# Kernel optimization log

Hardware: AMD Instinct MI355X
Metric: run time of the kernel (lower is better)

Reference implementation:

```python
import jax, jax.numpy as jnp
import numpy as np

T, B, N = 12, 2, 1024
M = B * N            # nodes per timestep (batch-flattened)
D_IN, D_H, D_T, D_O = 64, 128, 16, 32


def _linear_params(k, fin, fout):
    kw, kb = jax.random.split(k)
    s = 1.0 / np.sqrt(fin)
    w = jax.random.uniform(kw, (fin, fout), jnp.float32, -s, s)
    b = jax.random.uniform(kb, (fout,), jnp.float32, -s, s)
    return w, b


def setup_inputs() -> dict:
    key = jax.random.key(0)
    ks = jax.random.split(key, 12)
    x = jax.random.normal(ks[0], (T, M, D_IN), jnp.float32)
    A = (jax.random.uniform(ks[1], (T, M, M)) < 0.01).astype(jnp.float32)
    A = A * (1.0 - jnp.eye(M, dtype=jnp.float32))  # no self-loops in raw adjacency
    ego_mask = jax.random.randint(ks[2], (B, T, N), 0, 2).astype(bool)
    gcn1_w, gcn1_b = _linear_params(ks[3], D_IN, D_H)
    gcn2_w, gcn2_b = _linear_params(ks[4], D_H, D_H)
    time_w, time_b = _linear_params(ks[5], 1, D_T)
    q_w, q_b = _linear_params(ks[6], D_H + D_T, D_H)
    k_w, k_b = _linear_params(ks[7], D_H + D_T, D_H)
    v_w, v_b = _linear_params(ks[8], D_H + D_T, D_H)
    o_w, o_b = _linear_params(ks[9], D_H, D_H)
    fc_w, fc_b = _linear_params(ks[10], D_H, D_O)
    return dict(x=x, A=A, ego_mask=ego_mask,
                gcn1_w=gcn1_w, gcn1_b=gcn1_b, gcn2_w=gcn2_w, gcn2_b=gcn2_b,
                time_w=time_w, time_b=time_b,
                q_w=q_w, q_b=q_b, k_w=k_w, k_b=k_b, v_w=v_w, v_b=v_b,
                o_w=o_w, o_b=o_b, fc_w=fc_w, fc_b=fc_b)


def _forward(x, A, ego_mask, gcn1_w, gcn1_b, gcn2_w, gcn2_b, time_w, time_b,
             q_w, q_b, k_w, k_b, v_w, v_b, o_w, o_b, fc_w, fc_b):
    # [B,T,N] -> [T, B*N], as in mask.permute(1,0,2).reshape(T,-1)
    mask = ego_mask.transpose(1, 0, 2).reshape(T, M)
    tvals = jnp.arange(T, dtype=jnp.float32)

    def step(_, inp):
        xt, At, mt, tv = inp  # [M,D_IN], [M,M], [M] bool, scalar
        m = mt.astype(xt.dtype)
        # restrict adjacency to masked subgraph; GCNConv adds self-loops
        A_hat = At * (m[:, None] * m[None, :]) + jnp.diag(m)
        deg = A_hat.sum(axis=0)  # in-degree per target (PyG gcn_norm on col)
        nrm = jnp.where(deg > 0, 1.0 / jnp.sqrt(jnp.maximum(deg, 1e-12)), 0.0)

        def gcn(h, w, b):
            # out[i] = nrm[i] * sum_j A_hat[j,i] * nrm[j] * (hW)[j] + b
            return (A_hat.T @ ((h @ w) * nrm[:, None])) * nrm[:, None] + b

        h = jax.nn.relu(gcn(xt, gcn1_w, gcn1_b))
        h = jax.nn.relu(gcn(h, gcn2_w, gcn2_b))
        # t_vec = sin(Linear(1,D_T)(t)) -- identical for all nodes
        t_vec = jnp.sin(tv * time_w[0] + time_b)  # [D_T]
        xtc = jnp.concatenate([h, jnp.broadcast_to(t_vec, (M, D_T))], axis=-1)
        Q = xtc @ q_w + q_b
        K = xtc @ k_w + k_b
        V = xtc @ v_w + v_b
        scores = (Q @ K.T) * (1.0 / np.sqrt(D_H))  # [M,M]
        scores = jnp.where(mt[None, :], scores, -1e9)  # keys restricted to mask
        agg = jax.nn.softmax(scores, axis=-1) @ V
        out = ((agg @ o_w + o_b) @ fc_w + fc_b) * m[:, None]  # scatter-back == mask
        return None, out

    _, outs = jax.lax.scan(step, None, (x, A, mask, tvals))  # [T,M,D_O]
    return outs.reshape(T, B, N, D_O).transpose(1, 2, 0, 3)  # [B,N,T,D_O]


def reference(x, A, ego_mask, gcn1_w, gcn1_b, gcn2_w, gcn2_b, time_w, time_b,
              q_w, q_b, k_w, k_b, v_w, v_b, o_w, o_b, fc_w, fc_b):
    return _forward(x, A, ego_mask, gcn1_w, gcn1_b, gcn2_w, gcn2_b, time_w,
                    time_b, q_w, q_b, k_w, k_b, v_w, v_b, o_w, o_b, fc_w, fc_b)
```

## Files before the change

### kernel.cpp

```cpp
#include <hip/hip_runtime.h>
#include <stdint.h>

#define TT   12
#define BB   2
#define NN   1024
#define MM   2048
#define TM   24576
#define DIN  64
#define DH   128
#define DOUT 32
#define CAP  64
#define NSPL 4
#define OUTSZ 786432

typedef __attribute__((ext_vector_type(8))) short short8;
typedef __attribute__((ext_vector_type(4))) short short4v;
typedef __attribute__((ext_vector_type(4))) float f32x4;

#define MFMA(a,b,c) __builtin_amdgcn_mfma_f32_16x16x32_bf16((a),(b),(c),0,0,0)

__device__ __forceinline__ float bf2f(unsigned short u){
  union { uint32_t i; float f; } x; x.i = ((uint32_t)u) << 16; return x.f;
}
__device__ __forceinline__ unsigned short f2bf(float f){
  union { float f; uint32_t i; } x; x.f = f;
  uint32_t u = x.i + 0x7FFFu + ((x.i >> 16) & 1u);
  return (unsigned short)(u >> 16);
}
__device__ __forceinline__ float LD(const void* p, size_t i, int mode){
  return mode ? ((const float*)p)[i] : bf2f(((const unsigned short*)p)[i]);
}
__device__ __forceinline__ short8 ldx8(const void* x, size_t off, int md){
  if(md){
    const float4* xf = (const float4*)((const float*)x + off);
    float4 a = xf[0], b = xf[1];
    short8 o;
    o[0]=(short)f2bf(a.x); o[1]=(short)f2bf(a.y); o[2]=(short)f2bf(a.z); o[3]=(short)f2bf(a.w);
    o[4]=(short)f2bf(b.x); o[5]=(short)f2bf(b.y); o[6]=(short)f2bf(b.z); o[7]=(short)f2bf(b.w);
    return o;
  }
  return *(const short8*)((const unsigned short*)x + off);
}

__global__ void k_fill(float* __restrict__ out, int n, float val){
  int i = blockIdx.x*blockDim.x + threadIdx.x;
  if(i < n) out[i] = val;
}

__global__ void k_detect2(const unsigned short* __restrict__ x,
                          const unsigned char* __restrict__ eg,
                          int* __restrict__ dtf, int* __restrict__ flag,
                          int* __restrict__ nact){
  if(blockIdx.x == 0){
    __shared__ int cnt_s;
    if(threadIdx.x==0) cnt_s = 0;
    if(threadIdx.x < TT) nact[threadIdx.x] = 0;
    __syncthreads();
    int c = 0;
    for(int i=threadIdx.x; i<6144; i+=blockDim.x){
      unsigned short h = x[i*2];
      unsigned e = (h >> 7) & 0xFF;
      if(h==0 || (e >= 0x60 && e <= 0x9F)) c++;
    }
    atomicAdd(&cnt_s, c);
    __syncthreads();
    if(threadIdx.x==0) *dtf = (cnt_s > 4000) ? 0 : 1;
  } else {
    __shared__ int pres_s, ge2_s;
    if(threadIdx.x==0){ pres_s=0; ge2_s=0; }
    __syncthreads();
    int pres=0, ge2=0;
    for(int i=threadIdx.x; i<24576; i+=blockDim.x){
      unsigned v = eg[i];
      if(v){ pres |= 1 << (i & 7); if(v >= 2u) ge2 = 1; }
    }
    if(pres) atomicOr(&pres_s, pres);
    if(ge2)  atomicOr(&ge2_s, 1);
    __syncthreads();
    if(threadIdx.x==0){
      int pr = pres_s, g2 = ge2_s, mode;
      if(!g2){
        if((pr & ~0x01) == 0)      mode = 4;
        else if((pr & ~0x11) == 0) mode = 0;
        else                       mode = 1;
      } else {
        if((pr & ~0xC0) == 0)      mode = 5;
        else if((pr & ~0xCC) == 0) mode = 3;
        else                       mode = 2;
      }
      *flag = mode;
    }
  }
}

__global__ void k_mask(const void* __restrict__ egom, const int* __restrict__ flag,
                       int* __restrict__ cnt, int* __restrict__ nact,
                       int* __restrict__ aidx, int* __restrict__ inv,
                       float* __restrict__ out){
  int idx = blockIdx.x*blockDim.x + threadIdx.x;
  out[idx] = 0.f;
  if(idx >= TM) return;
  int t = idx / MM, node = idx % MM;
  int b = node / NN, n = node % NN;
  int src = (b*TT + t)*NN + n;
  int mode = *flag;
  int v;
  if(mode==0)      v = ((const int*)egom)[src] != 0;
  else if(mode==1) v = ((const unsigned char*)egom)[src] != 0;
  else if(mode==2) v = ((const unsigned short*)egom)[src] != 0;
  else if(mode==3) v = ((const float*)egom)[src] != 0.f;
  else if(mode==4) v = ((const long long*)egom)[src] != 0;
  else             v = ((const double*)egom)[src] != 0.0;
  cnt[idx] = 0;
  unsigned long long bal = __ballot(v != 0);
  int lane = threadIdx.x & 63;
  int base = 0;
  if(lane == 0 && bal) base = atomicAdd(&nact[t], __popcll(bal));
  base = __shfl(base, 0, 64);
  int ic = -1;
  if(v){
    int pfx = __popcll(bal & ((1ULL << lane) - 1ULL));
    ic = base + pfx;
    aidx[(size_t)t*MM + ic] = node;
  }
  inv[idx] = ic;
}

__global__ void k_prepw(
  const void* __restrict__ w1, const void* __restrict__ w2,
  const void* __restrict__ qw, const void* __restrict__ kw, const void* __restrict__ vw,
  const void* __restrict__ qb0, const void* __restrict__ kb0, const void* __restrict__ vb0,
  const void* __restrict__ ow, const void* __restrict__ ob,
  const void* __restrict__ fw, const void* __restrict__ fb,
  const void* __restrict__ tw, const void* __restrict__ tb,
  const void* __restrict__ b1, const void* __restrict__ b2,
  const int* __restrict__ dtf,
  unsigned short* __restrict__ W1t, unsigned short* __restrict__ W2t,
  unsigned short* __restrict__ Wqt, unsigned short* __restrict__ Wkt,
  unsigned short* __restrict__ Wvt, unsigned short* __restrict__ Wct,
  float* __restrict__ qbf, float* __restrict__ kbf, float* __restrict__ vbf,
  float* __restrict__ bcf, float* __restrict__ b1f, float* __restrict__ b2f)
{
  const int md = *dtf;
  int id = blockIdx.x*blockDim.x + threadIdx.x;
  if(id < 8192){
    int n=id&127, k2=id>>7; W1t[n*64+k2]=f2bf(LD(w1,(size_t)k2*128+n,md)); return; }
  id -= 8192;
  if(id < 16384){ int n=id&127,k2=id>>7; W2t[n*128+k2]=f2bf(LD(w2,(size_t)k2*128+n,md)); return; }
  id -= 16384;
  if(id < 16384){ int n=id&127,k2=id>>7; Wqt[n*128+k2]=f2bf(LD(qw,(size_t)k2*128+n,md)); return; }
  id -= 16384;
  if(id < 16384){ int n=id&127,k2=id>>7; Wkt[n*128+k2]=f2bf(LD(kw,(size_t)k2*128+n,md)); return; }
  id -= 16384;
  if(id < 16384){ int n=id&127,k2=id>>7; Wvt[n*128+k2]=f2bf(LD(vw,(size_t)k2*128+n,md)); return; }
  id -= 16384;
  if(id < 4096){
    int oc=id&31, c=id>>5; float s=0.f;
    for(int r=0;r<128;r++) s += LD(ow,(size_t)c*128+r,md)*LD(fw,(size_t)r*32+oc,md);
    Wct[oc*128+c]=f2bf(s); return;
  }
  id -= 4096;
  if(id < 32){
    float s = LD(fb,id,md);
    for(int r=0;r<128;r++) s += LD(ob,r,md)*LD(fw,(size_t)r*32+id,md);
    bcf[id]=s; return;
  }
  id -= 32;
  if(id < 4608){
    int which = id/1536, rem=id%1536, t=rem/128, n=rem%128;
    const void* W  = which==0?qw:(which==1?kw:vw);
    const void* Bs = which==0?qb0:(which==1?kb0:vb0);
    float s = LD(Bs,n,md);
    for(int d=0;d<16;d++){
      float tv = sinf((float)t*LD(tw,d,md) + LD(tb,d,md));
      s += tv * LD(W,(size_t)(128+d)*128+n,md);
    }
    float* dst = which==0?qbf:(which==1?kbf:vbf);
    dst[t*128+n]=s; return;
  }
  id -= 4608;
  if(id < 256){
    if(id<128) b1f[id] = LD(b1,id,md);
    else       b2f[id-128] = LD(b2,id-128,md);
    return;
  }
}

__global__ __launch_bounds__(256) void k_edges(const void* __restrict__ A,
    const int* __restrict__ dtf, const int* __restrict__ inv,
    int* __restrict__ cnt, int* __restrict__ edges){
  int id = blockIdx.x*blockDim.x + threadIdx.x;
  int seg = id & 63; int row = id >> 6;
  int t = row / MM;
  int jc = inv[row];
  if(jc < 0) return;
  const int* invt = inv + (size_t)t*MM;
  int* cb = cnt + (size_t)t*MM;
  int* eb = edges + (size_t)t*MM*CAP;
  if(*dtf){
    const float4* p4 = (const float4*)((const float*)A + (size_t)row*MM + seg*32);
    #pragma unroll
    for(int u=0;u<8;u++){
      float4 v = p4[u];
      float wd[4]={v.x,v.y,v.z,v.w};
      #pragma unroll
      for(int q=0;q<4;q++){
        if(wd[q]!=0.f){
          int ibc = invt[seg*32 + u*4 + q];
          if(ibc >= 0){ int s=atomicAdd(&cb[ibc],1); if(s<CAP) eb[(size_t)ibc*CAP+s]=jc; }
        }
      }
    }
  } else {
    const uint4* p4 = (const uint4*)((const unsigned short*)A + (size_t)row*MM + seg*32);
    #pragma unroll
    for(int u=0;u<4;u++){
      uint4 v = p4[u];
      unsigned wd[4]={v.x,v.y,v.z,v.w};
      #pragma unroll
      for(int q=0;q<4;q++){
        int ib = seg*32 + u*8 + q*2;
        if(wd[q] & 0xFFFFu){
          int ibc = invt[ib];
          if(ibc >= 0){ int s=atomicAdd(&cb[ibc],1); if(s<CAP) eb[(size_t)ibc*CAP+s]=jc; }
        }
        if(wd[q] >> 16){
          int ibc = invt[ib+1];
          if(ibc >= 0){ int s=atomicAdd(&cb[ibc],1); if(s<CAP) eb[(size_t)ibc*CAP+s]=jc; }
        }
      }
    }
  }
}

__global__ __launch_bounds__(256) void k_gemm_x(const void* __restrict__ x,
    const int* __restrict__ dtf, const int* __restrict__ nact,
    const int* __restrict__ aidx, const unsigned short* __restrict__ Wt,
    float* __restrict__ g)
{
  const int tile = blockIdx.x*64;
  const int t = tile / MM, il = tile % MM;
  const int na = nact[t];
  if(il >= ((na+63)&~63)) return;
  const int md = *dtf;
  const int tid=threadIdx.x, wv=tid>>6, lane=tid&63, l15=lane&15, quad=lane>>4;
  const int r0 = tile + (wv>>1)*32;
  const int c0 = (wv&1)*64;
  short8 bf[2][4];
  #pragma unroll
  for(int kk=0;kk<2;kk++)
    #pragma unroll
    for(int nt=0;nt<4;nt++)
      bf[kk][nt] = *(const short8*)(Wt + (size_t)(c0+nt*16+l15)*DIN + kk*32 + quad*8);
  const int il0 = (r0 % MM) + l15, il1 = (r0 % MM) + 16 + l15;
  const int n0 = aidx[(size_t)t*MM + (il0 < na ? il0 : 0)];
  const int n1 = aidx[(size_t)t*MM + (il1 < na ? il1 : 0)];
  const size_t xb0 = ((size_t)t*MM + n0)*DIN;
  const size_t xb1 = ((size_t)t*MM + n1)*DIN;
  f32x4 z = {0.f,0.f,0.f,0.f};
  f32x4 acc[2][4];
  #pragma unroll
  for(int i=0;i<2;i++){ acc[i][0]=z; acc[i][1]=z; acc[i][2]=z; acc[i][3]=z; }
  #pragma unroll
  for(int kk=0;kk<2;kk++){
    short8 a0 = ldx8(x, xb0 + kk*32 + quad*8, md);
    short8 a1 = ldx8(x, xb1 + kk*32 + quad*8, md);
    #pragma unroll
    for(int nt=0;nt<4;nt++){
      acc[0][nt]=MFMA(a0,bf[kk][nt],acc[0][nt]);
      acc[1][nt]=MFMA(a1,bf[kk][nt],acc[1][nt]);
    }
  }
  #pragma unroll
  for(int mt=0;mt<2;mt++)
    #pragma unroll
    for(int nt=0;nt<4;nt++){
      int col = c0+nt*16+l15;
      #pragma unroll
      for(int r=0;r<4;r++){
        int row = r0 + mt*16 + quad*4 + r;
        g[(size_t)row*DH + col] = acc[mt][nt][r];
      }
    }
}

__global__ __launch_bounds__(256) void k_gemm_h(const unsigned short* __restrict__ X,
    const unsigned short* __restrict__ Wt, float* __restrict__ g,
    const int* __restrict__ nact)
{
  const int tile = blockIdx.x*64;
  const int t = tile / MM, il = tile % MM;
  const int na = nact[t];
  if(il >= ((na+63)&~63)) return;
  const int tid=threadIdx.x, wv=tid>>6, lane=tid&63, l15=lane&15, quad=lane>>4;
  const int r0 = tile + (wv>>1)*32;
  const int c0 = (wv&1)*64;
  short8 bf[4][4];
  #pragma unroll
  for(int kk=0;kk<4;kk++)
    #pragma unroll
    for(int nt=0;nt<4;nt++)
      bf[kk][nt] = *(const short8*)(Wt + (size_t)(c0+nt*16+l15)*DH + kk*32 + quad*8);
  f32x4 z = {0.f,0.f,0.f,0.f};
  f32x4 acc[2][4];
  #pragma unroll
  for(int i=0;i<2;i++){ acc[i][0]=z; acc[i][1]=z; acc[i][2]=z; acc[i][3]=z; }
  #pragma unroll
  for(int kk=0;kk<4;kk++){
    short8 a0 = *(const short8*)(X + (size_t)(r0+l15)*DH    + kk*32 + quad*8);
    short8 a1 = *(const short8*)(X + (size_t)(r0+16+l15)*DH + kk*32 + quad*8);
    #pragma unroll
    for(int nt=0;nt<4;nt++){
      acc[0][nt]=MFMA(a0,bf[kk][nt],acc[0][nt]);
      acc[1][nt]=MFMA(a1,bf[kk][nt],acc[1][nt]);
    }
  }
  #pragma unroll
  for(int mt=0;mt<2;mt++)
    #pragma unroll
    for(int nt=0;nt<4;nt++){
      int col = c0+nt*16+l15;
      #pragma unroll
      for(int r=0;r<4;r++){
        int row = r0 + mt*16 + quad*4 + r;
        g[(size_t)row*DH + col] = acc[mt][nt][r];
      }
    }
}

__global__ __launch_bounds__(256) void k_gather(const float* __restrict__ g,
    const int* __restrict__ edges, const int* __restrict__ cnt,
    const int* __restrict__ nact, const float* __restrict__ bias,
    unsigned short* __restrict__ h)
{
  int wv = threadIdx.x>>6, lane = threadIdx.x&63;
  int gi = blockIdx.x*4 + wv;
  int t = gi / MM, ic = gi % MM;
  int na = nact[t];
  if(ic >= ((na+63)&~63)) return;
  if(ic >= na){
    h[(size_t)gi*DH + lane] = 0; h[(size_t)gi*DH + 64 + lane] = 0;
    return;
  }
  float a0=0.f, a1=0.f;
  int cn = cnt[gi]; if(cn>CAP) cn=CAP;
  const int* eb = edges + (size_t)gi*CAP;
  for(int e=0;e<cn;e++){
    int jc = eb[e];
    float nj = rsqrtf((float)cnt[(size_t)t*MM+jc] + 1.f);
    const float* gr = g + ((size_t)t*MM + jc)*DH;
    a0 += nj*gr[lane]; a1 += nj*gr[64+lane];
  }
  float ni = rsqrtf((float)cn + 1.f);
  const float* gs = g + (size_t)gi*DH;
  float h0 = ni*(a0 + ni*gs[lane])    + bias[lane];
  float h1 = ni*(a1 + ni*gs[64+lane]) + bias[64+lane];
  h0 = h0>0.f?h0:0.f; h1 = h1>0.f?h1:0.f;
  h[(size_t)gi*DH + lane]      = f2bf(h0);
  h[(size_t)gi*DH + 64 + lane] = f2bf(h1);
}

__global__ __launch_bounds__(256) void k_gemm_qkv(const unsigned short* __restrict__ X,
    const unsigned short* __restrict__ Wq, const unsigned short* __restrict__ Wk,
    const unsigned short* __restrict__ Wv,
    const float* __restrict__ qb, const float* __restrict__ kb, const float* __restrict__ vb,
    unsigned short* __restrict__ Qo, unsigned short* __restrict__ Ko,
    unsigned short* __restrict__ Vtc, const int* __restrict__ nact)
{
  const int tile = blockIdx.x*64;
  const int t = tile / MM, il = tile % MM;
  const int na = nact[t];
  if(il >= ((na+63)&~63)) return;
  const int which = blockIdx.z;
  const unsigned short* Wt = which==0?Wq:(which==1?Wk:Wv);
  const float* bias = which==0?qb:(which==1?kb:vb);
  const int tid=threadIdx.x, wv=tid>>6, lane=tid&63, l15=lane&15, quad=lane>>4;
  const int r0 = tile + (wv>>1)*32;
  const int c0 = (wv&1)*64;
  short8 bf[4][4];
  #pragma unroll
  for(int kk=0;kk<4;kk++)
    #pragma unroll
    for(int nt=0;nt<4;nt++)
      bf[kk][nt] = *(const short8*)(Wt + (size_t)(c0+nt*16+l15)*DH + kk*32 + quad*8);
  f32x4 z = {0.f,0.f,0.f,0.f};
  f32x4 acc[2][4];
  #pragma unroll
  for(int i=0;i<2;i++){ acc[i][0]=z; acc[i][1]=z; acc[i][2]=z; acc[i][3]=z; }
  #pragma unroll
  for(int kk=0;kk<4;kk++){
    short8 a0 = *(const short8*)(X + (size_t)(r0+l15)*DH    + kk*32 + quad*8);
    short8 a1 = *(const short8*)(X + (size_t)(r0+16+l15)*DH + kk*32 + quad*8);
    #pragma unroll
    for(int nt=0;nt<4;nt++){
      acc[0][nt]=MFMA(a0,bf[kk][nt],acc[0][nt]);
      acc[1][nt]=MFMA(a1,bf[kk][nt],acc[1][nt]);
    }
  }
  if(which < 2){
    unsigned short* o = which==0 ? Qo : Ko;
    #pragma unroll
    for(int mt=0;mt<2;mt++)
      #pragma unroll
      for(int nt=0;nt<4;nt++){
        int col = c0+nt*16+l15;
        float bb = bias[t*DH+col];
        #pragma unroll
        for(int r=0;r<4;r++){
          int row = r0 + mt*16 + quad*4 + r;
          o[(size_t)row*DH + col] = f2bf(acc[mt][nt][r] + bb);
        }
      }
  } else {
    #pragma unroll
    for(int mt=0;mt<2;mt++)
      #pragma unroll
      for(int nt=0;nt<4;nt++){
        int col = c0+nt*16+l15;
        float bb = bias[t*DH+col];
        int node0 = il + (wv>>1)*32 + mt*16 + quad*4;
        short4v pk;
        #pragma unroll
        for(int r=0;r<4;r++) pk[r] = (short)f2bf(acc[mt][nt][r] + bb);
        *(short4v*)(Vtc + ((size_t)t*DH + col)*MM + node0) = pk;
      }
  }
}

__global__ __launch_bounds__(64) void k_attn_split(
  const unsigned short* __restrict__ Q, const unsigned short* __restrict__ Kc,
  const unsigned short* __restrict__ Vtc, const int* __restrict__ nact,
  float* __restrict__ part, float* __restrict__ lpart)
{
  __shared__ short Pl[16][72];
  const int lane=threadIdx.x&63, l15=lane&15, quad=lane>>4;
  const int t = blockIdx.y;
  const int qbase = blockIdx.x*16;
  const int z = blockIdx.z;
  const float scale = 0.088388347648318447f;
  const int na = nact[t];
  if(qbase >= na) return;
  const int nkt = (na + 63) >> 6;
  const int chunk = (nkt + NSPL - 1) / NSPL;
  const int kt0 = z*chunk;
  int kt1 = kt0 + chunk; if(kt1 > nkt) kt1 = nkt;

  short8 bq[4];
  #pragma unroll
  for(int kk=0;kk<4;kk++)
    bq[kk] = *(const short8*)(Q + ((size_t)t*MM + qbase + l15)*DH + kk*32 + quad*8);

  f32x4 zz = {0.f,0.f,0.f,0.f};
  f32x4 accPV[8];
  #pragma unroll
  for(int i=0;i<8;i++) accPV[i]=zz;
  float l_run = 0.f;

  for(int kt=kt0; kt<kt1; kt++){
    const int key0 = kt*64;
    #pragma unroll
    for(int mt=0;mt<4;mt++){
      f32x4 s = zz;
      const unsigned short* Krow = Kc + ((size_t)t*MM + key0 + mt*16 + l15)*DH;
      #pragma unroll
      for(int kk=0;kk<4;kk++){
        short8 ak = *(const short8*)(Krow + kk*32 + quad*8);
        s = MFMA(ak, bq[kk], s);
      }
      short4v pk;
      #pragma unroll
      for(int r=0;r<4;r++){
        float sv = fminf(fmaxf(s[r]*scale, -15.f), 15.f);
        float valid = (key0 + mt*16 + quad*4 + r < na) ? 1.f : 0.f;
        float p = __expf(sv) * valid;
        pk[r] = (short)f2bf(p);
        l_run += bf2f((unsigned short)pk[r]);
      }
      *(short4v*)&Pl[l15][mt*16 + quad*4] = pk;
    }
    #pragma unroll
    for(int kk=0;kk<2;kk++){
      short8 ap = *(const short8*)&Pl[l15][kk*32 + quad*8];
      const unsigned short* Vb = Vtc + (size_t)t*DH*MM + key0 + kk*32 + quad*8;
      #pragma unroll
      for(int nt=0;nt<8;nt++){
        short8 bv = *(const short8*)(Vb + (size_t)(nt*16 + l15)*MM);
        accPV[nt] = MFMA(ap, bv, accPV[nt]);
      }
    }
  }
  l_run += __shfl_xor(l_run, 16, 64);
  l_run += __shfl_xor(l_run, 32, 64);

  const size_t pbase = (size_t)(z*TT + t)*MM + qbase;
  #pragma unroll
  for(int nt=0;nt<8;nt++)
    #pragma unroll
    for(int r=0;r<4;r++)
      part[(pbase + quad*4 + r)*128 + nt*16 + l15] = accPV[nt][r];
  if(lane < 16) lpart[pbase + lane] = l_run;
}

__global__ __launch_bounds__(64) void k_attn_fin(
  const float* __restrict__ part, const float* __restrict__ lpart,
  const int* __restrict__ aidx, const int* __restrict__ nact,
  const unsigned short* __restrict__ Wct, const float* __restrict__ bc,
  float* __restrict__ out)
{
  __shared__ short Al[16][136];
  __shared__ float lbuf[16];
  const int lane=threadIdx.x&63, l15=lane&15, quad=lane>>4;
  const int t = blockIdx.y, qbase = blockIdx.x*16;
  const int na = nact[t];
  if(qbase >= na) return;
  f32x4 acc4[8];
  f32x4 zz = {0.f,0.f,0.f,0.f};
  #pragma unroll
  for(int i=0;i<8;i++) acc4[i]=zz;
  #pragma unroll
  for(int s=0;s<NSPL;s++){
    const float* pb = part + ((size_t)(s*TT + t)*MM + qbase)*128;
    #pragma unroll
    for(int i=0;i<8;i++){
      int flat = i*64 + lane;
      int q = flat >> 5, c4 = (flat & 31) << 2;
      acc4[i] += *(const f32x4*)(pb + q*128 + c4);
    }
  }
  if(lane < 16){
    float ls = 0.f;
    #pragma unroll
    for(int s=0;s<NSPL;s++) ls += lpart[(size_t)(s*TT + t)*MM + qbase + lane];
    lbuf[lane] = ls;
  }
  #pragma unroll
  for(int i=0;i<8;i++){
    int flat = i*64 + lane;
    int q = flat >> 5, c4 = (flat & 31) << 2;
    short4v pk;
    #pragma unroll
    for(int r=0;r<4;r++){
      float av = fminf(fmaxf(acc4[i][r], -1e30f), 1e30f);
      pk[r] = (short)f2bf(av);
    }
    *(short4v*)&Al[q][c4] = pk;
  }
  __syncthreads();

  const int qc = qbase + l15;
  const bool qok = (qc < na);
  const float lsv = lbuf[l15];
  const float linv = (lsv > 0.f) ? 1.f/lsv : 0.f;
  const int node = aidx[(size_t)t*MM + (qok ? qc : 0)];
  #pragma unroll
  for(int mt2=0;mt2<2;mt2++){
    f32x4 d = zz;
    #pragma unroll
    for(int kk=0;kk<4;kk++){
      short8 aw = *(const short8*)(Wct + (size_t)(mt2*16+l15)*DH + kk*32 + quad*8);
      short8 bl = *(const short8*)&Al[l15][kk*32 + quad*8];
      d = MFMA(aw, bl, d);
    }
    f32x4 bcv = *(const f32x4*)(bc + mt2*16 + quad*4);
    f32x4 o4;
    #pragma unroll
    for(int r=0;r<4;r++) o4[r] = d[r]*linv + bcv[r];
    if(qok)
      *(f32x4*)(out + (size_t)node*(TT*DOUT) + (size_t)t*DOUT + mt2*16 + quad*4) = o4;
  }
}

extern "C" void kernel_launch(void* const* d_in, const int* in_sizes, int n_in,
                              void* d_out, int out_size, void* d_ws, size_t ws_size,
                              hipStream_t stream)
{
  float* outp = (float*)d_out;
  static const int EXP[19] = {1572864,50331648,24576,8192,128,16384,128,16,16,
                              18432,128,18432,128,18432,128,16384,128,4096,32};
  bool ok = (n_in >= 19) && (out_size == OUTSZ);
  if(ok) for(int i=0;i<19;i++) if(in_sizes[i] != EXP[i]) { ok = false; break; }
  if(!ok){
    k_fill<<<(out_size+255)/256,256,0,stream>>>(outp, out_size, 1000.f);
    return;
  }
  const void* x   = d_in[0];
  const void* A   = d_in[1];
  const void* eg  = d_in[2];
  const void* w1  = d_in[3];
  const void* b1  = d_in[4];
  const void* w2  = d_in[5];
  const void* b2  = d_in[6];
  const void* tw  = d_in[7];
  const void* tb  = d_in[8];
  const void* qw  = d_in[9];
  const void* qb0 = d_in[10];
  const void* kw  = d_in[11];
  const void* kb0 = d_in[12];
  const void* vw  = d_in[13];
  const void* vb0 = d_in[14];
  const void* ow  = d_in[15];
  const void* ob  = d_in[16];
  const void* fw  = d_in[17];
  const void* fb  = d_in[18];

  char* w = (char*)d_ws;
  size_t off = 0;
  auto alloc = [&](size_t sz)->char*{
    char* p = w + off; off = (off + sz + 255) & ~(size_t)255; return p; };
  int*   flag  = (int*)  alloc(4);
  int*   dtf   = (int*)  alloc(4);
  int*   nactb = (int*)  alloc(TT*4);
  int*   cnt   = (int*)  alloc((size_t)TM*4);
  int*   aidx  = (int*)  alloc((size_t)TM*4);
  int*   inv   = (int*)  alloc((size_t)TM*4);
  int*   edges = (int*)  alloc((size_t)TM*CAP*4);
  float* g     = (float*)alloc((size_t)TM*DH*4);
  unsigned short* h   = (unsigned short*)alloc((size_t)TM*DH*2);
  unsigned short* Vtc = (unsigned short*)alloc((size_t)TT*DH*MM*2);
  unsigned short* W1t = (unsigned short*)alloc(DH*DIN*2);
  unsigned short* W2t = (unsigned short*)alloc(DH*DH*2);
  unsigned short* Wqt = (unsigned short*)alloc(DH*DH*2);
  unsigned short* Wkt = (unsigned short*)alloc(DH*DH*2);
  unsigned short* Wvt = (unsigned short*)alloc(DH*DH*2);
  unsigned short* Wct = (unsigned short*)alloc(DOUT*DH*2);
  float* qbf = (float*)alloc(TT*DH*4);
  float* kbf = (float*)alloc(TT*DH*4);
  float* vbf = (float*)alloc(TT*DH*4);
  float* bcf = (float*)alloc(DOUT*4);
  float* b1f = (float*)alloc(DH*4);
  float* b2f = (float*)alloc(DH*4);
  float* part  = (float*)alloc((size_t)NSPL*TM*DH*4);
  float* lpart = (float*)alloc((size_t)NSPL*TM*4);
  if(off > ws_size){
    k_fill<<<(out_size+255)/256,256,0,stream>>>(outp, out_size, 500.f);
    return;
  }

  unsigned short* Qb = (unsigned short*)g;
  unsigned short* Kb = (unsigned short*)((char*)g + (size_t)TM*DH*2);

  k_detect2<<<2,256,0,stream>>>((const unsigned short*)x, (const unsigned char*)eg,
                                dtf, flag, nactb);
  k_mask<<<OUTSZ/256,256,0,stream>>>(eg, flag, cnt, nactb, aidx, inv, outp);
  k_prepw<<<(82720+255)/256,256,0,stream>>>(w1,w2,qw,kw,vw,qb0,kb0,vb0,ow,ob,fw,fb,tw,tb,
                                            b1,b2,dtf,
                                            W1t,W2t,Wqt,Wkt,Wvt,Wct,qbf,kbf,vbf,bcf,b1f,b2f);
  k_edges<<<TM*64/256,256,0,stream>>>(A, dtf, inv, cnt, edges);
  k_gemm_x<<<TM/64,256,0,stream>>>(x, dtf, nactb, aidx, W1t, g);
  k_gather<<<TM/4,256,0,stream>>>(g, edges, cnt, nactb, b1f, h);
  k_gemm_h<<<TM/64,256,0,stream>>>(h, W2t, g, nactb);
  k_gather<<<TM/4,256,0,stream>>>(g, edges, cnt, nactb, b2f, h);
  k_gemm_qkv<<<dim3(TM/64,1,3),256,0,stream>>>(h, Wqt,Wkt,Wvt, qbf,kbf,vbf, Qb,Kb,Vtc, nactb);
  k_attn_split<<<dim3(MM/16,TT,NSPL),64,0,stream>>>(Qb, Kb, Vtc, nactb, part, lpart);
  k_attn_fin<<<dim3(MM/16,TT),64,0,stream>>>(part, lpart, aidx, nactb, Wct, bcf, outp);
}
```

Before: 562.3 us.

## Share K/V tiles across four query waves via LDS in attention split kernel

The attention split kernel grows from one wave per 16 queries to a 256-thread block covering 64 queries. Each K and V tile is loaded cooperatively into shared memory once per key tile and reused by all four waves. Previously every wave read the same K/V tiles straight from global memory. This cuts redundant global/L2 traffic at the cost of two barriers per tile, more LDS, and fewer blocks.

```diff
diff --git a/kernel.cpp b/kernel.cpp
--- a/kernel.cpp
+++ b/kernel.cpp
@@ -427,19 +427,22 @@
   }
 }
 
-__global__ __launch_bounds__(64) void k_attn_split(
+__global__ __launch_bounds__(256) void k_attn_split(
   const unsigned short* __restrict__ Q, const unsigned short* __restrict__ Kc,
   const unsigned short* __restrict__ Vtc, const int* __restrict__ nact,
   float* __restrict__ part, float* __restrict__ lpart)
 {
-  __shared__ short Pl[16][72];
-  const int lane=threadIdx.x&63, l15=lane&15, quad=lane>>4;
-  const int t = blockIdx.y;
-  const int qbase = blockIdx.x*16;
-  const int z = blockIdx.z;
+  __shared__ unsigned short Kl[64][136];
+  __shared__ unsigned short Vl[128][72];
+  __shared__ short Pl[4][16][72];
+  const int tid=threadIdx.x, wv=tid>>6, lane=tid&63, l15=lane&15, quad=lane>>4;
+  const int t = blockIdx.y, z = blockIdx.z;
+  const int na = nact[t];
+  const int qblk = blockIdx.x*64;
+  if(qblk >= na) return;
+  const int qbase = qblk + wv*16;
+  const bool qact = (qbase < na);
   const float scale = 0.088388347648318447f;
-  const int na = nact[t];
-  if(qbase >= na) return;
   const int nkt = (na + 63) >> 6;
   const int chunk = (nkt + NSPL - 1) / NSPL;
   const int kt0 = z*chunk;
@@ -456,15 +459,31 @@
   for(int i=0;i<8;i++) accPV[i]=zz;
   float l_run = 0.f;
 
+  const int srow = tid >> 2, sseg = tid & 3;
+  const int vch  = tid >> 1, vhalf = tid & 1;
+
   for(int kt=kt0; kt<kt1; kt++){
     const int key0 = kt*64;
+    __syncthreads();
+    {
+      const unsigned short* gk = Kc + ((size_t)t*MM + key0 + srow)*DH + sseg*32;
+      short8* dst = (short8*)&Kl[srow][sseg*32];
+      #pragma unroll
+      for(int j=0;j<4;j++) dst[j] = *(const short8*)(gk + j*8);
+    }
+    {
+      const unsigned short* gv = Vtc + ((size_t)t*DH + vch)*MM + key0 + vhalf*32;
+      short8* dst = (short8*)&Vl[vch][vhalf*32];
+      #pragma unroll
+      for(int j=0;j<4;j++) dst[j] = *(const short8*)(gv + j*8);
+    }
+    __syncthreads();
     #pragma unroll
     for(int mt=0;mt<4;mt++){
       f32x4 s = zz;
-      const unsigned short* Krow = Kc + ((size_t)t*MM + key0 + mt*16 + l15)*DH;
       #pragma unroll
       for(int kk=0;kk<4;kk++){
-        short8 ak = *(const short8*)(Krow + kk*32 + quad*8);
+        short8 ak = *(const short8*)&Kl[mt*16+l15][kk*32 + quad*8];
         s = MFMA(ak, bq[kk], s);
       }
       short4v pk;
@@ -476,15 +495,14 @@
         pk[r] = (short)f2bf(p);
         l_run += bf2f((unsigned short)pk[r]);
       }
-      *(short4v*)&Pl[l15][mt*16 + quad*4] = pk;
+      *(short4v*)&Pl[wv][l15][mt*16 + quad*4] = pk;
     }
     #pragma unroll
     for(int kk=0;kk<2;kk++){
-      short8 ap = *(const short8*)&Pl[l15][kk*32 + quad*8];
-      const unsigned short* Vb = Vtc + (size_t)t*DH*MM + key0 + kk*32 + quad*8;
+      short8 ap = *(const short8*)&Pl[wv][l15][kk*32 + quad*8];
       #pragma unroll
       for(int nt=0;nt<8;nt++){
-        short8 bv = *(const short8*)(Vb + (size_t)(nt*16 + l15)*MM);
+        short8 bv = *(const short8*)&Vl[nt*16+l15][kk*32 + quad*8];
         accPV[nt] = MFMA(ap, bv, accPV[nt]);
       }
     }
@@ -492,13 +510,15 @@
   l_run += __shfl_xor(l_run, 16, 64);
   l_run += __shfl_xor(l_run, 32, 64);
 
-  const size_t pbase = (size_t)(z*TT + t)*MM + qbase;
-  #pragma unroll
-  for(int nt=0;nt<8;nt++)
-    #pragma unroll
-    for(int r=0;r<4;r++)
-      part[(pbase + quad*4 + r)*128 + nt*16 + l15] = accPV[nt][r];
-  if(lane < 16) lpart[pbase + lane] = l_run;
+  if(qact){
+    const size_t pbase = (size_t)(z*TT + t)*MM + qbase;
+    #pragma unroll
+    for(int nt=0;nt<8;nt++)
+      #pragma unroll
+      for(int r=0;r<4;r++)
+        part[(pbase + quad*4 + r)*128 + nt*16 + l15] = accPV[nt][r];
+    if(lane < 16) lpart[pbase + lane] = l_run;
+  }
 }
 
 __global__ __launch_bounds__(64) void k_attn_fin(
@@ -651,6 +671,6 @@
   k_gemm_h<<<TM/64,256,0,stream>>>(h, W2t, g, nactb);
   k_gather<<<TM/4,256,0,stream>>>(g, edges, cnt, nactb, b2f, h);
   k_gemm_qkv<<<dim3(TM/64,1,3),256,0,stream>>>(h, Wqt,Wkt,Wvt, qbf,kbf,vbf, Qb,Kb,Vtc, nactb);
-  k_attn_split<<<dim3(MM/16,TT,NSPL),64,0,stream>>>(Qb, Kb, Vtc, nactb, part, lpart);
+  k_attn_split<<<dim3(MM/64,TT,NSPL),256,0,stream>>>(Qb, Kb, Vtc, nactb, part, lpart);
   k_attn_fin<<<dim3(MM/16,TT),64,0,stream>>>(part, lpart, aidx, nactb, Wct, bcf, outp);
 }
```

Result: faster. 541.0 us (-3.8%).
